# Performance work log

Measured on AMD Instinct MI355X. Metric: run time of the kernel, lower is better.

Reference implementation:

```python
import jax, jax.numpy as jnp
import numpy as np

D_MODEL = 1024
N_HEADS = 16
D_HEAD = D_MODEL // N_HEADS
BLOCK = 2048
EPS = 1e-5


def layer_norm(x, w, b):
    mu = jnp.mean(x, axis=-1, keepdims=True)
    var = jnp.mean(jnp.square(x - mu), axis=-1, keepdims=True)
    return (x - mu) * jax.lax.rsqrt(var + EPS) * w + b


def setup_inputs() -> dict:
    key = jax.random.key(0)
    ks = jax.random.split(key, 8)
    d = D_MODEL
    s = 1.0 / np.sqrt(d)
    return {
        "x": jax.random.normal(ks[0], (2, 2048, d), dtype=jnp.float32),
        "ln1_w": jnp.ones((d,), jnp.float32),
        "ln1_b": jnp.zeros((d,), jnp.float32),
        "ln2_w": jnp.ones((d,), jnp.float32),
        "ln2_b": jnp.zeros((d,), jnp.float32),
        "qkv_w": jax.random.normal(ks[1], (3 * d, d), jnp.float32) * s,
        "o_w": jax.random.normal(ks[2], (d, d), jnp.float32) * s,
        "ffn_w1": jax.random.normal(ks[3], (4 * d, d), jnp.float32) * s,
        "ffn_b1": jnp.zeros((4 * d,), jnp.float32),
        "ffn_w2": jax.random.normal(ks[4], (d, 4 * d), jnp.float32) * (1.0 / np.sqrt(4 * d)),
        "ffn_b2": jnp.zeros((d,), jnp.float32),
    }


def reference(x, ln1_w, ln1_b, ln2_w, ln2_b, qkv_w, o_w, ffn_w1, ffn_b1, ffn_w2, ffn_b2):
    b, n, d = x.shape
    h = layer_norm(x, ln1_w, ln1_b)
    # qkv: (b, n, 3, H, Dh)
    qkv = (h @ qkv_w.T).reshape(b, n, 3, N_HEADS, D_HEAD)
    q, k, v = qkv[:, :, 0], qkv[:, :, 1], qkv[:, :, 2]  # (b, n, H, Dh)
    scale = 1.0 / np.sqrt(D_HEAD)
    s = jnp.einsum("bqhd,bkhd->bhqk", q, k) * scale
    mask = jnp.tril(jnp.ones((n, n), dtype=bool))
    s = jnp.where(mask, s, -jnp.inf)
    a = jax.nn.softmax(s, axis=-1)
    attn_out = jnp.einsum("bhqk,bkhd->bqhd", a, v).reshape(b, n, d)
    x = x + attn_out @ o_w.T
    h2 = layer_norm(x, ln2_w, ln2_b)
    ff = jax.nn.gelu(h2 @ ffn_w1.T + ffn_b1, approximate=False) @ ffn_w2.T + ffn_b2
    return x + ff
```

## Files before the change

### kernel.cpp

```cpp
#include <hip/hip_runtime.h>
#include <math.h>

#define D_MODEL 1024
#define N_HEADS 16
#define D_HEAD  64
#define SEQ     2048
#define BATCH   2
#define M_TOT   (BATCH*SEQ)
#define FFN_DIM 4096

typedef __attribute__((ext_vector_type(8))) short bf16x8;
typedef __attribute__((ext_vector_type(4))) float f32x4;
typedef __attribute__((ext_vector_type(8))) unsigned short u16x8;

__device__ __forceinline__ unsigned short f2bf(float f) {
  unsigned int u = __float_as_uint(f);
  return (unsigned short)((u + 0x7fffu + ((u >> 16) & 1u)) >> 16);
}
__device__ __forceinline__ float bf2f(unsigned short s) {
  return __uint_as_float(((unsigned int)s) << 16);
}

__device__ __forceinline__ void async_ld16(void* lds, const void* g) {
  __builtin_amdgcn_global_load_lds(
      (const __attribute__((address_space(1))) unsigned int*)g,
      (__attribute__((address_space(3))) unsigned int*)lds, 16, 0, 0);
}

__device__ __forceinline__ float gelu_exact(float x) {
  return 0.5f * x * (1.f + erff(x * 0.70710678118654752f));
}

__global__ __launch_bounds__(256) void cvt_all(const float* __restrict__ qkv_w,
    const float* __restrict__ o_w, const float* __restrict__ w1,
    const float* __restrict__ w2, unsigned short* __restrict__ dst) {
  const long MEGc = 1024*1024;
  long i = (long)(blockIdx.x*256 + threadIdx.x)*4;
  const float* src; long off;
  if (i < 3*MEGc)      { src = qkv_w; off = i; }
  else if (i < 4*MEGc) { src = o_w;  off = i - 3*MEGc; }
  else if (i < 8*MEGc) { src = w1;   off = i - 4*MEGc; }
  else                 { src = w2;   off = i - 8*MEGc; }
  float4 v = *(const float4*)(src + off);
  ushort4 o = { f2bf(v.x), f2bf(v.y), f2bf(v.z), f2bf(v.w) };
  *(ushort4*)(dst + i) = o;
}

__global__ __launch_bounds__(256) void ln_kernel(const float* __restrict__ x,
    const float* __restrict__ w, const float* __restrict__ b,
    unsigned short* __restrict__ out) {
  int row = blockIdx.x;
  const float* xr = x + (size_t)row * D_MODEL;
  int c = threadIdx.x * 4;
  float4 v = *(const float4*)(xr + c);
  float s = v.x + v.y + v.z + v.w;
  __shared__ float red[4];
  #pragma unroll
  for (int o = 32; o > 0; o >>= 1) s += __shfl_down(s, o, 64);
  int wave = threadIdx.x >> 6;
  if ((threadIdx.x & 63) == 0) red[wave] = s;
  __syncthreads();
  float mean = (red[0]+red[1]+red[2]+red[3]) * (1.f/D_MODEL);
  __syncthreads();
  float d0 = v.x-mean, d1 = v.y-mean, d2 = v.z-mean, d3 = v.w-mean;
  float s2 = d0*d0 + d1*d1 + d2*d2 + d3*d3;
  #pragma unroll
  for (int o = 32; o > 0; o >>= 1) s2 += __shfl_down(s2, o, 64);
  if ((threadIdx.x & 63) == 0) red[wave] = s2;
  __syncthreads();
  float var = (red[0]+red[1]+red[2]+red[3]) * (1.f/D_MODEL);
  float rs = rsqrtf(var + 1e-5f);
  float4 wv = *(const float4*)(w + c);
  float4 bv = *(const float4*)(b + c);
  ushort4 o = { f2bf(d0*rs*wv.x + bv.x), f2bf(d1*rs*wv.y + bv.y),
                f2bf(d2*rs*wv.z + bv.z), f2bf(d3*rs*wv.w + bv.w) };
  *(ushort4*)(out + (size_t)row*D_MODEL + c) = o;
}

__device__ __forceinline__ void swizzle_block(int nbx, int nby, int& bx, int& by) {
  int nb = nbx * nby;
  int bid = blockIdx.y * nbx + blockIdx.x;
  int chunk = nb >> 3;
  int bid2 = (bid & 7) * chunk + (bid >> 3);
  const int GM = 8;
  int ngroup = GM * nbx;
  int g = bid2 / ngroup, rem = bid2 % ngroup;
  by = g*GM + (rem % GM);
  bx = rem / GM;
}

template<int EPI, bool OBF, int BN>
__global__ __launch_bounds__(256) void gemm_mfma(
    const unsigned short* __restrict__ A, const unsigned short* __restrict__ Bt,
    float* __restrict__ Cf, unsigned short* __restrict__ Cb,
    const float* __restrict__ bias, const float* __restrict__ res,
    int M, int N, int K) {
  constexpr int BM = 128, BK = 32;
  constexpr int NI = (BN == 128) ? 4 : 2;
  __shared__ unsigned short As[2][BM*BK];
  __shared__ unsigned short Bs[2][BN*BK];
  int tid = threadIdx.x;
  int w = tid >> 6, l = tid & 63;
  int lg = l >> 4, lm = l & 15;
  int bx, by;
  swizzle_block(N/BN, M/BM, bx, by);
  int bm = by * BM, bn = bx * BN;
  int wm = (BN == 128) ? (w >> 1) * 64 : w * 32;
  int wn = (BN == 128) ? (w & 1) * 64 : 0;

  f32x4 acc[NI][4];
  #pragma unroll
  for (int i = 0; i < NI; ++i)
    #pragma unroll
    for (int j = 0; j < 4; ++j)
      acc[i][j] = (f32x4){0.f, 0.f, 0.f, 0.f};

  int fa0 = (2*w+0)*512 + l*8;
  int fa1 = (2*w+1)*512 + l*8;
  const unsigned short* a0 = A + (size_t)(bm + (fa0 >> 5))*K + (fa0 & 31);
  const unsigned short* a1 = A + (size_t)(bm + (fa1 >> 5))*K + (fa1 & 31);
  const unsigned short* b0;
  const unsigned short* b1 = nullptr;
  if (BN == 128) {
    b0 = Bt + (size_t)(bn + (fa0 >> 5))*K + (fa0 & 31);
    b1 = Bt + (size_t)(bn + (fa1 >> 5))*K + (fa1 & 31);
  } else {
    int fb0 = w*512 + l*8;
    b0 = Bt + (size_t)(bn + (fb0 >> 5))*K + (fb0 & 31);
  }

  auto stage = [&](int buf, int k0) {
    async_ld16(&As[buf][(2*w+0)*512], a0 + k0);
    async_ld16(&As[buf][(2*w+1)*512], a1 + k0);
    if (BN == 128) {
      async_ld16(&Bs[buf][(2*w+0)*512], b0 + k0);
      async_ld16(&Bs[buf][(2*w+1)*512], b1 + k0);
    } else {
      async_ld16(&Bs[buf][w*512], b0 + k0);
    }
  };

  int aoff = (wm + lm)*BK + lg*8;
  int boff = (wn + lm)*BK + lg*8;

  stage(0, 0);
  int niter = K / BK;
  for (int kt = 0; kt < niter; ++kt) {
    __syncthreads();
    if (kt + 1 < niter) stage((kt+1) & 1, (kt+1)*BK);
    int buf = kt & 1;
    bf16x8 af[NI], bfr[4];
    #pragma unroll
    for (int i = 0; i < NI; ++i) af[i]  = *(const bf16x8*)&As[buf][aoff + i*512];
    #pragma unroll
    for (int j = 0; j < 4; ++j)  bfr[j] = *(const bf16x8*)&Bs[buf][boff + j*512];
    #pragma unroll
    for (int i = 0; i < NI; ++i)
      #pragma unroll
      for (int j = 0; j < 4; ++j)
        acc[i][j] = __builtin_amdgcn_mfma_f32_16x16x32_bf16(af[i], bfr[j], acc[i][j], 0, 0, 0);
  }

  #pragma unroll
  for (int i = 0; i < NI; ++i) {
    #pragma unroll
    for (int j = 0; j < 4; ++j) {
      int col = bn + wn + j*16 + lm;
      #pragma unroll
      for (int r = 0; r < 4; ++r) {
        int row = bm + wm + i*16 + lg*4 + r;
        float v = acc[i][j][r];
        if (EPI == 1) v = gelu_exact(v + bias[col]);
        if (EPI == 2) v += res[(size_t)row*N + col];
        if (EPI == 3) v += bias[col] + res[(size_t)row*N + col];
        if (OBF) Cb[(size_t)row*N + col] = f2bf(v);
        else     Cf[(size_t)row*N + col] = v;
      }
    }
  }
}

__global__ __launch_bounds__(256) void vtrans_kernel(
    const unsigned short* __restrict__ qkvb, unsigned short* __restrict__ vT) {
  __shared__ unsigned short T[64*72];
  int nt = blockIdx.x, h = blockIdx.y, b = blockIdx.z;
  int tid = threadIdx.x;
  const unsigned short* vb = qkvb + (size_t)(b*SEQ)*(3*D_MODEL) + 2*D_MODEL + h*D_HEAD;
  #pragma unroll
  for (int it = 0; it < 2; ++it) {
    int idx = tid + it*256;
    int r = idx >> 3, c8 = (idx & 7)*8;
    *(u16x8*)&T[r*72 + c8] = *(const u16x8*)(vb + (size_t)(nt*64 + r)*(3*D_MODEL) + c8);
  }
  __syncthreads();
  unsigned short* vto = vT + ((size_t)(b*N_HEADS + h)*D_HEAD)*SEQ + nt*64;
  #pragma unroll
  for (int it = 0; it < 2; ++it) {
    int idx = tid + it*256;
    int d = idx >> 3, s8 = (idx & 7)*8;
    u16x8 o;
    #pragma unroll
    for (int i = 0; i < 8; ++i) o[i] = T[(s8+i)*72 + d];
    *(u16x8*)(vto + (size_t)d*SEQ + s8) = o;
  }
}

#define ATT_PAD 72
__device__ __forceinline__ void attn_step(
    const bf16x8* aq, float* m_i, float* l_i, f32x4* acc_o,
    const unsigned short* __restrict__ Ks, const unsigned short* __restrict__ Vt,
    unsigned short* __restrict__ pw, int lg, int lm, int qoff, bool diag) {
  f32x4 sacc[4];
  #pragma unroll
  for (int j = 0; j < 4; ++j) sacc[j] = (f32x4){0.f, 0.f, 0.f, 0.f};
  #pragma unroll
  for (int s = 0; s < 2; ++s)
    #pragma unroll
    for (int j = 0; j < 4; ++j)
      sacc[j] = __builtin_amdgcn_mfma_f32_16x16x32_bf16(
          aq[s], *(const bf16x8*)&Ks[(j*16+lm)*ATT_PAD + s*32 + lg*8], sacc[j], 0, 0, 0);
  if (diag) {
    #pragma unroll
    for (int j = 0; j < 4; ++j)
      #pragma unroll
      for (int r = 0; r < 4; ++r)
        if (j*16 + lm > qoff + lg*4 + r) sacc[j][r] = -INFINITY;
  }
  float alpha[4];
  #pragma unroll
  for (int r = 0; r < 4; ++r) {
    float rm = fmaxf(fmaxf(sacc[0][r], sacc[1][r]), fmaxf(sacc[2][r], sacc[3][r]));
    #pragma unroll
    for (int o = 1; o < 16; o <<= 1) rm = fmaxf(rm, __shfl_xor(rm, o));
    float mn = fmaxf(m_i[r], rm);
    alpha[r] = __expf(m_i[r] - mn);
    float rsum = 0.f;
    #pragma unroll
    for (int j = 0; j < 4; ++j) {
      float p = __expf(sacc[j][r] - mn);
      sacc[j][r] = p; rsum += p;
    }
    #pragma unroll
    for (int o = 1; o < 16; o <<= 1) rsum += __shfl_xor(rsum, o);
    l_i[r] = l_i[r]*alpha[r] + rsum;
    m_i[r] = mn;
  }
  #pragma unroll
  for (int j = 0; j < 4; ++j)
    #pragma unroll
    for (int r = 0; r < 4; ++r)
      pw[(lg*4 + r)*ATT_PAD + j*16 + lm] = f2bf(sacc[j][r]);
  #pragma unroll
  for (int j = 0; j < 4; ++j)
    #pragma unroll
    for (int r = 0; r < 4; ++r)
      acc_o[j][r] *= alpha[r];
  #pragma unroll
  for (int s = 0; s < 2; ++s) {
    bf16x8 ap = *(const bf16x8*)&pw[lm*ATT_PAD + s*32 + lg*8];
    #pragma unroll
    for (int j = 0; j < 4; ++j)
      acc_o[j] = __builtin_amdgcn_mfma_f32_16x16x32_bf16(
          ap, *(const bf16x8*)&Vt[(j*16+lm)*ATT_PAD + s*32 + lg*8], acc_o[j], 0, 0, 0);
  }
}

__global__ __launch_bounds__(256) void attn_mfma_kernel(
    const unsigned short* __restrict__ qkvb, const unsigned short* __restrict__ vT,
    unsigned short* __restrict__ out) {
  __shared__ unsigned short Ks[64*ATT_PAD];
  __shared__ unsigned short Vt[64*ATT_PAD];
  __shared__ unsigned short Pw[4][16*ATT_PAD];

  int pr = blockIdx.x, h = blockIdx.y, b = blockIdx.z;
  int qtH = 31 - pr, qtL = pr;
  int tid = threadIdx.x;
  int w = tid >> 6, l = tid & 63;
  int lg = l >> 4, lm = l & 15;

  const size_t rs3 = 3*D_MODEL;
  const unsigned short* qb  = qkvb + (size_t)(b*SEQ)*rs3 + h*D_HEAD;
  const unsigned short* kb  = qb + D_MODEL;
  const unsigned short* vtb = vT + ((size_t)(b*N_HEADS + h)*D_HEAD)*SEQ;

  bf16x8 aqH[2], aqL[2];
  int qrH = qtH*64 + w*16 + lm, qrL = qtL*64 + w*16 + lm;
  #pragma unroll
  for (int s = 0; s < 2; ++s) {
    u16x8 tH = *(const u16x8*)(qb + (size_t)qrH*rs3 + s*32 + lg*8);
    u16x8 tL = *(const u16x8*)(qb + (size_t)qrL*rs3 + s*32 + lg*8);
    bf16x8 rH, rL;
    #pragma unroll
    for (int i = 0; i < 8; ++i) {
      rH[i] = (short)f2bf(bf2f(tH[i]) * 0.125f);
      rL[i] = (short)f2bf(bf2f(tL[i]) * 0.125f);
    }
    aqH[s] = rH; aqL[s] = rL;
  }

  float mH[4], lH[4], mL[4], lL[4];
  f32x4 oH[4], oL[4];
  #pragma unroll
  for (int r = 0; r < 4; ++r) { mH[r] = -INFINITY; lH[r] = 0.f; mL[r] = -INFINITY; lL[r] = 0.f; }
  #pragma unroll
  for (int j = 0; j < 4; ++j) { oH[j] = (f32x4){0.f,0.f,0.f,0.f}; oL[j] = (f32x4){0.f,0.f,0.f,0.f}; }

  unsigned short* pw = &Pw[w][0];

  for (int kt = 0; kt <= qtH; ++kt) {
    __syncthreads();
    #pragma unroll
    for (int it = 0; it < 2; ++it) {
      int idx = tid + it*256;
      int r = idx >> 3, c8 = (idx & 7)*8;
      *(u16x8*)&Ks[r*ATT_PAD + c8] = *(const u16x8*)(kb + (size_t)(kt*64 + r)*rs3 + c8);
      *(u16x8*)&Vt[r*ATT_PAD + c8] = *(const u16x8*)(vtb + (size_t)r*SEQ + kt*64 + c8);
    }
    __syncthreads();
    attn_step(aqH, mH, lH, oH, Ks, Vt, pw, lg, lm, w*16, kt == qtH);
    if (kt <= qtL)
      attn_step(aqL, mL, lL, oL, Ks, Vt, pw, lg, lm, w*16, kt == qtL);
  }

  #pragma unroll
  for (int r = 0; r < 4; ++r) {
    float invH = 1.f / lH[r], invL = 1.f / lL[r];
    int qH = qtH*64 + w*16 + lg*4 + r;
    int qL = qtL*64 + w*16 + lg*4 + r;
    #pragma unroll
    for (int j = 0; j < 4; ++j) {
      out[((size_t)(b*SEQ + qH))*D_MODEL + h*D_HEAD + j*16 + lm] = f2bf(oH[j][r]*invH);
      out[((size_t)(b*SEQ + qL))*D_MODEL + h*D_HEAD + j*16 + lm] = f2bf(oL[j][r]*invL);
    }
  }
}

extern "C" void kernel_launch(void* const* d_in, const int* in_sizes, int n_in,
                              void* d_out, int out_size, void* d_ws, size_t ws_size,
                              hipStream_t stream) {
  const float* x      = (const float*)d_in[0];
  const float* ln1_w  = (const float*)d_in[1];
  const float* ln1_b  = (const float*)d_in[2];
  const float* ln2_w  = (const float*)d_in[3];
  const float* ln2_b  = (const float*)d_in[4];
  const float* qkv_w  = (const float*)d_in[5];
  const float* o_w    = (const float*)d_in[6];
  const float* ffn_w1 = (const float*)d_in[7];
  const float* ffn_b1 = (const float*)d_in[8];
  const float* ffn_w2 = (const float*)d_in[9];
  const float* ffn_b2 = (const float*)d_in[10];
  float* out = (float*)d_out;
  float* ws  = (float*)d_ws;

  const size_t MEG = 1024*1024;
  unsigned short* wqkv = (unsigned short*)ws;
  unsigned short* wo   = wqkv + 3*MEG;
  unsigned short* w1   = wo   + 1*MEG;
  unsigned short* w2   = w1   + 4*MEG;
  unsigned short* hbf    = (unsigned short*)(ws + 6*MEG);
  unsigned short* attnbf = (unsigned short*)(ws + 8*MEG);
  float* x1  = ws + 10*MEG;
  unsigned short* qkvb = (unsigned short*)(ws + 14*MEG);
  unsigned short* ffbf = (unsigned short*)(ws + 14*MEG);
  unsigned short* vT   = (unsigned short*)(ws + 22*MEG);

  cvt_all<<<12*MEG/1024, 256, 0, stream>>>(qkv_w, o_w, ffn_w1, ffn_w2, wqkv);
  ln_kernel<<<M_TOT, 256, 0, stream>>>(x, ln1_w, ln1_b, hbf);
  gemm_mfma<0,true,128><<<dim3(3*D_MODEL/128, M_TOT/128), 256, 0, stream>>>(
      hbf, wqkv, nullptr, qkvb, nullptr, nullptr, M_TOT, 3*D_MODEL, D_MODEL);
  vtrans_kernel<<<dim3(SEQ/64, N_HEADS, BATCH), 256, 0, stream>>>(qkvb, vT);
  attn_mfma_kernel<<<dim3(16, N_HEADS, BATCH), 256, 0, stream>>>(qkvb, vT, attnbf);
  gemm_mfma<2,false,64><<<dim3(D_MODEL/64, M_TOT/128), 256, 0, stream>>>(
      attnbf, wo, x1, nullptr, nullptr, x, M_TOT, D_MODEL, D_MODEL);
  ln_kernel<<<M_TOT, 256, 0, stream>>>(x1, ln2_w, ln2_b, hbf);
  gemm_mfma<1,true,128><<<dim3(FFN_DIM/128, M_TOT/128), 256, 0, stream>>>(
      hbf, w1, nullptr, ffbf, ffn_b1, nullptr, M_TOT, FFN_DIM, D_MODEL);
  gemm_mfma<3,false,64><<<dim3(D_MODEL/64, M_TOT/128), 256, 0, stream>>>(
      ffbf, w2, out, nullptr, ffn_b2, x1, M_TOT, D_MODEL, FFN_DIM);
}
```

Measured before the change: 391.3 us.

## Widen attention KV tile to 128 keys per step with chunk-level causal skip

```diff
diff --git a/kernel.cpp b/kernel.cpp
--- a/kernel.cpp
+++ b/kernel.cpp
@@ -16,6 +16,9 @@
 __device__ __forceinline__ unsigned short f2bf(float f) {
   unsigned int u = __float_as_uint(f);
   return (unsigned short)((u + 0x7fffu + ((u >> 16) & 1u)) >> 16);
+}
+__device__ __forceinline__ unsigned short f2bf_trunc(float f) {
+  return (unsigned short)(__float_as_uint(f) >> 16);
 }
 __device__ __forceinline__ float bf2f(unsigned short s) {
   return __uint_as_float(((unsigned int)s) << 16);
@@ -205,72 +208,91 @@
   }
 }
 
-#define ATT_PAD 72
-__device__ __forceinline__ void attn_step(
+#define KS_PAD 72
+#define VT_PAD 136
+__device__ __forceinline__ void attn_step128(
     const bf16x8* aq, float* m_i, float* l_i, f32x4* acc_o,
     const unsigned short* __restrict__ Ks, const unsigned short* __restrict__ Vt,
-    unsigned short* __restrict__ pw, int lg, int lm, int qoff, bool diag) {
-  f32x4 sacc[4];
-  #pragma unroll
-  for (int j = 0; j < 4; ++j) sacc[j] = (f32x4){0.f, 0.f, 0.f, 0.f};
-  #pragma unroll
-  for (int s = 0; s < 2; ++s)
-    #pragma unroll
-    for (int j = 0; j < 4; ++j)
-      sacc[j] = __builtin_amdgcn_mfma_f32_16x16x32_bf16(
-          aq[s], *(const bf16x8*)&Ks[(j*16+lm)*ATT_PAD + s*32 + lg*8], sacc[j], 0, 0, 0);
-  if (diag) {
-    #pragma unroll
-    for (int j = 0; j < 4; ++j)
-      #pragma unroll
-      for (int r = 0; r < 4; ++r)
-        if (j*16 + lm > qoff + lg*4 + r) sacc[j][r] = -INFINITY;
-  }
+    unsigned short* __restrict__ pw, int lg, int lm, int qbase, int kvbase,
+    bool diag) {
+  f32x4 sacc[2][4];
+  #pragma unroll
+  for (int cj = 0; cj < 2; ++cj) {
+    bool skip = diag && (kvbase + cj*64 > qbase + 15);
+    if (skip) {
+      #pragma unroll
+      for (int j = 0; j < 4; ++j)
+        sacc[cj][j] = (f32x4){-INFINITY, -INFINITY, -INFINITY, -INFINITY};
+    } else {
+      #pragma unroll
+      for (int j = 0; j < 4; ++j) sacc[cj][j] = (f32x4){0.f, 0.f, 0.f, 0.f};
+      #pragma unroll
+      for (int s = 0; s < 2; ++s)
+        #pragma unroll
+        for (int j = 0; j < 4; ++j)
+          sacc[cj][j] = __builtin_amdgcn_mfma_f32_16x16x32_bf16(
+              aq[s], *(const bf16x8*)&Ks[(cj*64+j*16+lm)*KS_PAD + s*32 + lg*8],
+              sacc[cj][j], 0, 0, 0);
+      if (diag) {
+        #pragma unroll
+        for (int j = 0; j < 4; ++j)
+          #pragma unroll
+          for (int r = 0; r < 4; ++r)
+            if (kvbase + cj*64 + j*16 + lm > qbase + lg*4 + r)
+              sacc[cj][j][r] = -INFINITY;
+      }
+    }
+  }
+
   float alpha[4];
   #pragma unroll
   for (int r = 0; r < 4; ++r) {
-    float rm = fmaxf(fmaxf(sacc[0][r], sacc[1][r]), fmaxf(sacc[2][r], sacc[3][r]));
+    float rm = -INFINITY;
+    #pragma unroll
+    for (int cj = 0; cj < 2; ++cj)
+      #pragma unroll
+      for (int j = 0; j < 4; ++j)
+        rm = fmaxf(rm, sacc[cj][j][r]);
     #pragma unroll
     for (int o = 1; o < 16; o <<= 1) rm = fmaxf(rm, __shfl_xor(rm, o));
     float mn = fmaxf(m_i[r], rm);
     alpha[r] = __expf(m_i[r] - mn);
     float rsum = 0.f;
     #pragma unroll
-    for (int j = 0; j < 4; ++j) {
-      float p = __expf(sacc[j][r] - mn);
-      sacc[j][r] = p; rsum += p;
-    }
+    for (int cj = 0; cj < 2; ++cj)
+      #pragma unroll
+      for (int j = 0; j < 4; ++j) {
+        float p = __expf(sacc[cj][j][r] - mn);
+        pw[(lg*4 + r)*VT_PAD + cj*64 + j*16 + lm] = f2bf_trunc(p);
+        rsum += p;
+      }
     #pragma unroll
     for (int o = 1; o < 16; o <<= 1) rsum += __shfl_xor(rsum, o);
     l_i[r] = l_i[r]*alpha[r] + rsum;
     m_i[r] = mn;
   }
-  #pragma unroll
-  for (int j = 0; j < 4; ++j)
-    #pragma unroll
-    for (int r = 0; r < 4; ++r)
-      pw[(lg*4 + r)*ATT_PAD + j*16 + lm] = f2bf(sacc[j][r]);
+
   #pragma unroll
   for (int j = 0; j < 4; ++j)
     #pragma unroll
     for (int r = 0; r < 4; ++r)
       acc_o[j][r] *= alpha[r];
   #pragma unroll
-  for (int s = 0; s < 2; ++s) {
-    bf16x8 ap = *(const bf16x8*)&pw[lm*ATT_PAD + s*32 + lg*8];
+  for (int ks = 0; ks < 4; ++ks) {
+    bf16x8 ap = *(const bf16x8*)&pw[lm*VT_PAD + ks*32 + lg*8];
     #pragma unroll
     for (int j = 0; j < 4; ++j)
       acc_o[j] = __builtin_amdgcn_mfma_f32_16x16x32_bf16(
-          ap, *(const bf16x8*)&Vt[(j*16+lm)*ATT_PAD + s*32 + lg*8], acc_o[j], 0, 0, 0);
+          ap, *(const bf16x8*)&Vt[(j*16+lm)*VT_PAD + ks*32 + lg*8], acc_o[j], 0, 0, 0);
   }
 }
 
 __global__ __launch_bounds__(256) void attn_mfma_kernel(
     const unsigned short* __restrict__ qkvb, const unsigned short* __restrict__ vT,
     unsigned short* __restrict__ out) {
-  __shared__ unsigned short Ks[64*ATT_PAD];
-  __shared__ unsigned short Vt[64*ATT_PAD];
-  __shared__ unsigned short Pw[4][16*ATT_PAD];
+  __shared__ unsigned short Ks[128*KS_PAD];
+  __shared__ unsigned short Vt[64*VT_PAD];
+  __shared__ unsigned short Pw[4][16*VT_PAD];
 
   int pr = blockIdx.x, h = blockIdx.y, b = blockIdx.z;
   int qtH = 31 - pr, qtL = pr;
@@ -306,20 +328,27 @@
   for (int j = 0; j < 4; ++j) { oH[j] = (f32x4){0.f,0.f,0.f,0.f}; oL[j] = (f32x4){0.f,0.f,0.f,0.f}; }
 
   unsigned short* pw = &Pw[w][0];
-
-  for (int kt = 0; kt <= qtH; ++kt) {
+  int nstH = qtH/2 + 1, nstL = qtL/2 + 1;
+
+  for (int s = 0; s < nstH; ++s) {
+    int kvbase = s*128;
     __syncthreads();
     #pragma unroll
-    for (int it = 0; it < 2; ++it) {
+    for (int it = 0; it < 4; ++it) {
       int idx = tid + it*256;
       int r = idx >> 3, c8 = (idx & 7)*8;
-      *(u16x8*)&Ks[r*ATT_PAD + c8] = *(const u16x8*)(kb + (size_t)(kt*64 + r)*rs3 + c8);
-      *(u16x8*)&Vt[r*ATT_PAD + c8] = *(const u16x8*)(vtb + (size_t)r*SEQ + kt*64 + c8);
+      *(u16x8*)&Ks[r*KS_PAD + c8] = *(const u16x8*)(kb + (size_t)(kvbase + r)*rs3 + c8);
+    }
+    #pragma unroll
+    for (int it = 0; it < 4; ++it) {
+      int idx = tid + it*256;
+      int d = idx >> 4, c8 = (idx & 15)*8;
+      *(u16x8*)&Vt[d*VT_PAD + c8] = *(const u16x8*)(vtb + (size_t)d*SEQ + kvbase + c8);
     }
     __syncthreads();
-    attn_step(aqH, mH, lH, oH, Ks, Vt, pw, lg, lm, w*16, kt == qtH);
-    if (kt <= qtL)
-      attn_step(aqL, mL, lL, oL, Ks, Vt, pw, lg, lm, w*16, kt == qtL);
+    attn_step128(aqH, mH, lH, oH, Ks, Vt, pw, lg, lm, qtH*64 + w*16, kvbase, s == nstH-1);
+    if (s < nstL)
+      attn_step128(aqL, mL, lL, oL, Ks, Vt, pw, lg, lm, qtL*64 + w*16, kvbase, s == nstL-1);
   }
 
   #pragma unroll
```

New measurement: 465.2 us. +18.9%, slower.
